# Performance work log

Hardware: AMD Instinct MI355X
Metric: run time of the kernel (lower is better)

Reference implementation:

```python
import jax, jax.numpy as jnp
import numpy as np

B, L, D = 16384, 50, 64      # nodes, history length, embed_dim
NU, NI, NR = 100000, 100000, 5


def setup_inputs() -> dict:
    key = jax.random.key(0)
    ks = jax.random.split(key, 16)
    s = 0.05
    return {
        "nodes": jax.random.randint(ks[0], (B,), 0, NU),
        "history_uv": jax.random.randint(ks[1], (B, L), 0, NI),
        "history_r": jax.random.randint(ks[2], (B, L), 0, NR),
        "v2e_w": jax.random.normal(ks[3], (NI, D), jnp.float32) * s,
        "u2e_w": jax.random.normal(ks[4], (NU, D), jnp.float32) * s,
        "r2e_w": jax.random.normal(ks[5], (NR, D), jnp.float32) * s,
        "w_r1_w": jax.random.normal(ks[6], (2 * D, D), jnp.float32) * s,
        "w_r1_b": jnp.zeros((D,), jnp.float32),
        "w_r2_w": jax.random.normal(ks[7], (D, D), jnp.float32) * s,
        "w_r2_b": jnp.zeros((D,), jnp.float32),
        "att1_w": jax.random.normal(ks[8], (2 * D, D), jnp.float32) * s,
        "att1_b": jnp.zeros((D,), jnp.float32),
        "att2_w": jax.random.normal(ks[9], (D, D), jnp.float32) * s,
        "att2_b": jnp.zeros((D,), jnp.float32),
        "att3_w": jax.random.normal(ks[10], (D, 1), jnp.float32) * s,
        "att3_b": jnp.zeros((1,), jnp.float32),
    }


def reference(nodes, history_uv, history_r, v2e_w, u2e_w, r2e_w,
              w_r1_w, w_r1_b, w_r2_w, w_r2_b,
              att1_w, att1_b, att2_w, att2_b, att3_w, att3_b):
    # Gather neighbor (item) and rating embeddings: [B, L, D]
    e_uv = v2e_w[history_uv]
    e_r = r2e_w[history_r]
    uv_rep = u2e_w[nodes]                      # [B, D] self (user) embedding
    # 2-layer MLP on concatenated (item, rating) embeddings
    x = jnp.concatenate([e_uv, e_r], axis=-1)  # [B, L, 2D]
    h = jax.nn.relu(x @ w_r1_w + w_r1_b)
    o_history = jax.nn.relu(h @ w_r2_w + w_r2_b)  # [B, L, D]
    # Attention over neighbors (GraphRec Attention, dropout off in eval)
    a = jnp.concatenate(
        [o_history, jnp.broadcast_to(uv_rep[:, None, :], o_history.shape)], axis=-1)
    a = jax.nn.relu(a @ att1_w + att1_b)
    a = jax.nn.relu(a @ att2_w + att2_b)
    logits = (a @ att3_w + att3_b)[..., 0]     # [B, L]
    att = jax.nn.softmax(logits, axis=-1)      # softmax over history dim
    # Attention-weighted sum of neighbor representations
    return jnp.einsum('bl,bld->bd', att, o_history)  # [B, D]
```

## Files before the change

kernel.cpp:

```cpp
#include <hip/hip_runtime.h>
#include <math.h>

#define NB 16384
#define LH 50
#define D  64

#define TBF_OFF 49152
#define UB_OFF  65536
#define P1_OFF  4259840

typedef _Float16 half2v __attribute__((ext_vector_type(2)));
typedef _Float16 half8  __attribute__((ext_vector_type(8)));
typedef float    f32x16 __attribute__((ext_vector_type(16)));
typedef unsigned int u32;

#define MFMA(a, b, c) __builtin_amdgcn_mfma_f32_32x32x16_f16((a), (b), (c), 0, 0, 0)


__device__ __forceinline__ u32 pack2(float a, float b) {
    half2v h; h[0] = (_Float16)a; h[1] = (_Float16)b;
    return __builtin_bit_cast(u32, h);
}
__device__ __forceinline__ half8 mk8(u32 a, u32 b, u32 c, u32 d) {
    uint4 t = make_uint4(a, b, c, d);
    return __builtin_bit_cast(half8, t);
}
__device__ __forceinline__ half8 cvt8(const float* __restrict__ p) {
    float4 u = *(const float4*)p;
    float4 v = *(const float4*)(p + 4);
    return mk8(pack2(u.x, u.y), pack2(u.z, u.w), pack2(v.x, v.y), pack2(v.z, v.w));
}
__device__ __forceinline__ half8 addrelu8(half8 a, half8 r) {
    half8 s = a + r;
    #pragma unroll
    for (int j = 0; j < 8; ++j) s[j] = s[j] > (_Float16)0 ? s[j] : (_Float16)0;
    return s;
}

__device__ __forceinline__ void xform_tile(const f32x16& t, int hv, half8& f0, half8& f1) {
    u32 p[8], rp[8];
    #pragma unroll
    for (int q = 0; q < 8; ++q) p[q] = pack2(fmaxf(t[2*q], 0.f), fmaxf(t[2*q+1], 0.f));
    #pragma unroll
    for (int q = 0; q < 8; ++q) rp[q] = (u32)__shfl_xor((int)p[q], 32, 64);
    f0 = hv ? mk8(rp[2], rp[3], p[2], p[3]) : mk8(p[0], p[1], rp[0], rp[1]);
    f1 = hv ? mk8(rp[6], rp[7], p[6], p[7]) : mk8(p[4], p[5], rp[4], rp[5]);
}

__device__ __forceinline__ f32x16 ldbias(const float* tb, int hv, int mt) {
    const float4* p = (const float4*)tb + hv*8 + mt*4;
    f32x16 r;
    #pragma unroll
    for (int q = 0; q < 4; ++q) {
        float4 v = p[q];
        r[4*q] = v.x; r[4*q+1] = v.y; r[4*q+2] = v.z; r[4*q+3] = v.w;
    }
    return r;
}

__device__ __forceinline__ half8 mkw(const float* __restrict__ W, int ks, int mt,
                                     int hv, int m) {
    half8 r;
    #pragma unroll
    for (int j = 0; j < 8; ++j)
        r[j] = (_Float16)W[(ks*16 + hv*8 + j)*64 + mt*32 + m];
    return r;
}

__global__ __launch_bounds__(256) void prep_all(
    const int*   __restrict__ nodes,
    const float* __restrict__ v2e, const float* __restrict__ u2e,
    const float* __restrict__ r2e,
    const float* __restrict__ w1,  const float* __restrict__ b1,
    const float* __restrict__ w2,  const float* __restrict__ b2,
    const float* __restrict__ wa1, const float* __restrict__ ba1,
    const float* __restrict__ wa2, const float* __restrict__ ba2,
    const float* __restrict__ wa3,
    _Float16* __restrict__ wsh, float* __restrict__ tbf,
    float* __restrict__ UB, _Float16* __restrict__ P1h) {
    const int blk = blockIdx.x;
    const int lane = threadIdx.x & 63;
    const int n = lane & 31, hv = lane >> 5;

    if (blk < 782) {
        const int tile = blk*4 + (threadIdx.x >> 6);
        if (tile >= 3125) return;
        const int item = tile*32 + n;
        half8 bf[4];
        #pragma unroll
        for (int ks = 0; ks < 4; ++ks)
            bf[ks] = cvt8(v2e + (size_t)item*64 + ks*16 + hv*8);
        f32x16 a0, a1;
        #pragma unroll
        for (int q = 0; q < 16; ++q) { a0[q] = 0.f; a1[q] = 0.f; }
        #pragma unroll
        for (int ks = 0; ks < 4; ++ks) {
            a0 = MFMA(mkw(w1, ks, 0, hv, n), bf[ks], a0);
            a1 = MFMA(mkw(w1, ks, 1, hv, n), bf[ks], a1);
        }
        u32 dw[16];
        #pragma unroll
        for (int q = 0; q < 8; ++q) dw[q]     = pack2(a0[2*q], a0[2*q+1]);
        #pragma unroll
        for (int q = 0; q < 8; ++q) dw[8 + q] = pack2(a1[2*q], a1[2*q+1]);
        uint4* dst = (uint4*)(P1h + (size_t)item*64 + hv*32);
        dst[0] = make_uint4(dw[0],  dw[1],  dw[2],  dw[3]);
        dst[1] = make_uint4(dw[4],  dw[5],  dw[6],  dw[7]);
        dst[2] = make_uint4(dw[8],  dw[9],  dw[10], dw[11]);
        dst[3] = make_uint4(dw[12], dw[13], dw[14], dw[15]);
        return;
    }
    if (blk < 910) {
        const int tile = (blk - 782)*4 + (threadIdx.x >> 6);
        const int s = tile*32 + n;
        const int nid = nodes[s];
        half8 bf[4];
        #pragma unroll
        for (int ks = 0; ks < 4; ++ks)
            bf[ks] = cvt8(u2e + (size_t)nid*64 + ks*16 + hv*8);
        f32x16 a0, a1;
        #pragma unroll
        for (int q = 0; q < 16; ++q) {
            a0[q] = ba1[(q & 3) + 8*(q >> 2) + 4*hv];
            a1[q] = ba1[32 + (q & 3) + 8*(q >> 2) + 4*hv];
        }
        const float* wup = wa1 + 64*64;
        #pragma unroll
        for (int ks = 0; ks < 4; ++ks) {
            a0 = MFMA(mkw(wup, ks, 0, hv, n), bf[ks], a0);
            a1 = MFMA(mkw(wup, ks, 1, hv, n), bf[ks], a1);
        }
        float4* dst = (float4*)(UB + (size_t)s*64 + hv*32);
        #pragma unroll
        for (int q = 0; q < 4; ++q) {
            dst[q]     = make_float4(a0[4*q], a0[4*q+1], a0[4*q+2], a0[4*q+3]);
            dst[4 + q] = make_float4(a1[4*q], a1[4*q+1], a1[4*q+2], a1[4*q+3]);
        }
        return;
    }
    if (blk < 958) {
        const int idx = (blk - 910)*256 + threadIdx.x;
        const int j = idx & 7, l2 = (idx >> 3) & 63;
        const int hv2 = l2 >> 5, m31 = l2 & 31;
        const int f = (idx >> 9) & 7, ks = f & 3, mt = f >> 2;
        const int sec = idx >> 12;
        const int tau = ks*16 + hv2*8 + j;
        float v;
        if (sec == 0) {
            const int thv = (tau >> 5) & 1, tmt = (tau >> 4) & 1, i = tau & 15;
            const int feat = tmt*32 + (i & 3) + 8*(i >> 2) + 4*thv;
            v = w2[feat*64 + mt*32 + m31];
        }
        else if (sec == 1) v = wa1[tau*64 + mt*32 + m31];
        else               v = wa2[tau*64 + mt*32 + m31];
        wsh[idx] = (_Float16)v;
        return;
    }
    if (blk == 958) {
        if (threadIdx.x < 64) {
            const int t = threadIdx.x;
            const int thv = t >> 5, r = t & 31, mtt = r >> 4, i = r & 15;
            const int feat = mtt*32 + (i & 3) + 8*(i >> 2) + 4*thv;
            tbf[t]       = b2[feat];
            tbf[64 + t]  = ba2[feat];
            tbf[128 + t] = wa3[feat];
        }
        return;
    }
    {
        _Float16* R1h = (_Float16*)(tbf + 192);
        #pragma unroll 1
        for (int base = 0; base < 320; base += 256) {
            const int o = base + (int)threadIdx.x;
            if (o < 320) {
                const int rr = o >> 6, tt = o & 63;
                const int thv = tt >> 5, r5 = tt & 31, mtt = r5 >> 4, i = r5 & 15;
                const int feat = mtt*32 + (i & 3) + 8*(i >> 2) + 4*thv;
                float acc = b1[feat];
                for (int k = 0; k < 64; ++k)
                    acc += r2e[rr*64 + k] * w1[(64 + k)*64 + feat];
                R1h[rr*64 + tt] = (_Float16)acc;
            }
        }
    }
}

__global__ __launch_bounds__(256, 4) void uv_main(
    const int*   __restrict__ huv,
    const int*   __restrict__ hr,
    const _Float16* __restrict__ P1h,
    const float* __restrict__ UB,
    const _Float16* __restrict__ wsh,
    const float* __restrict__ tbf,
    float*       __restrict__ out) {
    __shared__ _Float16 lw[12288];
    __shared__ float    ltb[192];
    __shared__ _Float16 lr1[5*72];
    const int tid = threadIdx.x;

    {
        const uint4* src = (const uint4*)wsh;
        uint4* dst = (uint4*)lw;
        #pragma unroll
        for (int i = 0; i < 6; ++i) dst[tid + 256*i] = src[tid + 256*i];
        if (tid < 48) ((uint4*)ltb)[tid] = ((const uint4*)tbf)[tid];
        if (tid < 40) {
            const int r = tid >> 3, q = tid & 7;
            ((uint4*)lr1)[r*9 + q] = ((const uint4*)(tbf + 192))[tid];
        }
    }
    __syncthreads();

    const int lane = tid & 63;
    const int w = tid >> 6;
    const int b = blockIdx.x * 4 + w;
    const int n = lane & 31, hv = lane >> 5;

    #define G8(base, f) (*(const half8*)(lw + (base) + ((f)*64 + lane)*8))

    const int t1   = (32 + n < LH) ? 32 + n : LH - 1;
    const int row0 = huv[b*LH + n];
    const int row1 = huv[b*LH + t1];
    const int ir0  = hr[b*LH + n];
    const int ir1  = hr[b*LH + t1];

    half8 bf[2][4];
    #pragma unroll
    for (int ks = 0; ks < 4; ++ks) {
        half8 p0 = *(const half8*)(P1h + (size_t)row0*64 + ks*16 + hv*8);
        half8 p1 = *(const half8*)(P1h + (size_t)row1*64 + ks*16 + hv*8);
        half8 r0 = *(const half8*)(lr1 + ir0*72 + ks*16 + hv*8);
        half8 r1 = *(const half8*)(lr1 + ir1*72 + ks*16 + hv*8);
        bf[0][ks] = addrelu8(p0, r0);
        bf[1][ks] = addrelu8(p1, r1);
    }

    half8 of[2][4];
    #pragma unroll
    for (int mt = 0; mt < 2; ++mt) {
        f32x16 a0 = ldbias(ltb, hv, mt);
        f32x16 a1 = ldbias(ltb, hv, mt);
        #pragma unroll
        for (int ks = 0; ks < 4; ++ks) {
            half8 wv = G8(0, mt*4 + ks);
            a0 = MFMA(wv, bf[0][ks], a0);
            a1 = MFMA(wv, bf[1][ks], a1);
        }
        xform_tile(a0, hv, of[0][mt*2], of[0][mt*2 + 1]);
        xform_tile(a1, hv, of[1][mt*2], of[1][mt*2 + 1]);
    }

    const float* ubrow = UB + (size_t)b * 64;
    half8 af[2][4];
    #pragma unroll
    for (int mt = 0; mt < 2; ++mt) {
        f32x16 a0 = ldbias(ubrow, hv, mt);
        f32x16 a1 = ldbias(ubrow, hv, mt);
        #pragma unroll
        for (int ks = 0; ks < 4; ++ks) {
            half8 wv = G8(4096, mt*4 + ks);
            a0 = MFMA(wv, of[0][ks], a0);
            a1 = MFMA(wv, of[1][ks], a1);
        }
        xform_tile(a0, hv, af[0][mt*2], af[0][mt*2 + 1]);
        xform_tile(a1, hv, af[1][mt*2], af[1][mt*2 + 1]);
    }

    float lg0 = 0.f, lg1 = 0.f;
    #pragma unroll
    for (int mt = 0; mt < 2; ++mt) {
        f32x16 c0, c1v;
        {
            const f32x16 bc = ldbias(ltb + 64, hv, mt);
            half8 wv = G8(8192, mt*4 + 0);
            c0  = MFMA(wv, af[0][0], bc);
            c1v = MFMA(wv, af[1][0], bc);
        }
        #pragma unroll
        for (int ks = 1; ks < 4; ++ks) {
            half8 wv = G8(8192, mt*4 + ks);
            c0  = MFMA(wv, af[0][ks], c0);
            c1v = MFMA(wv, af[1][ks], c1v);
        }
        #pragma unroll
        for (int q = 0; q < 4; ++q) {
            float4 w3 = ((const float4*)(ltb + 128))[hv*8 + mt*4 + q];
            lg0 += fmaxf(c0[4*q], 0.f)*w3.x + fmaxf(c0[4*q+1], 0.f)*w3.y
                 + fmaxf(c0[4*q+2], 0.f)*w3.z + fmaxf(c0[4*q+3], 0.f)*w3.w;
            lg1 += fmaxf(c1v[4*q], 0.f)*w3.x + fmaxf(c1v[4*q+1], 0.f)*w3.y
                 + fmaxf(c1v[4*q+2], 0.f)*w3.z + fmaxf(c1v[4*q+3], 0.f)*w3.w;
        }
    }
    lg0 += __shfl_xor(lg0, 32, 64);
    lg1 += __shfl_xor(lg1, 32, 64);
    if (32 + n >= LH) lg1 = -1e30f;

    float mx = fmaxf(lg0, lg1);
    #pragma unroll
    for (int off = 16; off >= 1; off >>= 1) mx = fmaxf(mx, __shfl_xor(mx, off, 64));
    const float e0 = __expf(lg0 - mx);
    const float e1 = __expf(lg1 - mx);
    float s = e0 + e1;
    #pragma unroll
    for (int off = 16; off >= 1; off >>= 1) s += __shfl_xor(s, off, 64);
    const float at0 = e0 / s, at1 = e1 / s;

    float cur[32];
    #pragma unroll
    for (int ks = 0; ks < 4; ++ks)
        #pragma unroll
        for (int j = 0; j < 8; ++j)
            cur[ks*8 + j] = at0 * (float)of[0][ks][j] + at1 * (float)of[1][ks][j];
    #pragma unroll
    for (int k = 0; k < 5; ++k) {
        const int d = 1 << k, mybit = (lane >> k) & 1, half = 16 >> k;
        #pragma unroll
        for (int j2 = 0; j2 < 16; ++j2) {
            if (j2 < half) {
                float sel  = mybit ? cur[2*j2]     : cur[2*j2 + 1];
                float got  = __shfl_xor(sel, d, 64);
                float keep = mybit ? cur[2*j2 + 1] : cur[2*j2];
                cur[j2] = keep + got;
            }
        }
    }
    const int feat = ((lane >> 3) & 3)*16 + hv*8 + (lane & 7);
    __builtin_nontemporal_store(cur[0], out + (size_t)b * D + feat);
    #undef G8
}

extern "C" void kernel_launch(void* const* d_in, const int* in_sizes, int n_in,
                              void* d_out, int out_size, void* d_ws, size_t ws_size,
                              hipStream_t stream) {
    const int*   nodes      = (const int*)  d_in[0];
    const int*   history_uv = (const int*)  d_in[1];
    const int*   history_r  = (const int*)  d_in[2];
    const float* v2e        = (const float*)d_in[3];
    const float* u2e        = (const float*)d_in[4];
    const float* r2e        = (const float*)d_in[5];
    const float* w1         = (const float*)d_in[6];
    const float* b1         = (const float*)d_in[7];
    const float* w2         = (const float*)d_in[8];
    const float* b2         = (const float*)d_in[9];
    const float* wa1        = (const float*)d_in[10];
    const float* ba1        = (const float*)d_in[11];
    const float* wa2        = (const float*)d_in[12];
    const float* ba2        = (const float*)d_in[13];
    const float* wa3        = (const float*)d_in[14];
    float* out = (float*)d_out;

    _Float16* wsh = (_Float16*)d_ws;
    float*    tbf = (float*)((char*)d_ws + TBF_OFF);
    float*    UB  = (float*)((char*)d_ws + UB_OFF);
    _Float16* P1h = (_Float16*)((char*)d_ws + P1_OFF);

    prep_all<<<960, 256, 0, stream>>>(nodes, v2e, u2e, r2e, w1, b1, w2, b2,
                                      wa1, ba1, wa2, ba2, wa3, wsh, tbf, UB, P1h);
    uv_main<<<NB/4, 256, 0, stream>>>(history_uv, history_r,
                                      P1h, UB, wsh, tbf, out);
}
```

Before: 170.4 us.

## Permute feature order in weights to drop cross-lane shuffles; use 512-thread blocks

Precomputed weights, the P1 table and the output index are re-permuted so the MFMA accumulator layout can feed the next MFMA directly. This removes the __shfl_xor lane-swap in each tile transform. The main kernel also moves from 4 to 8 waves per block, so each block does half as many shared-memory weight loads per node and the grid halves. Correctness depends on every permutation matching. Launch bounds of 512×4 may raise register pressure.

```diff
diff --git a/kernel.cpp b/kernel.cpp
--- a/kernel.cpp
+++ b/kernel.cpp
@@ -17,6 +17,11 @@
 #define MFMA(a, b, c) __builtin_amdgcn_mfma_f32_32x32x16_f16((a), (b), (c), 0, 0, 0)
 
 
+__device__ __forceinline__ int featn(int s) {
+    const int ks = s >> 4, hvv = (s >> 3) & 1, j = s & 7;
+    return (ks >> 1)*32 + (ks & 1)*16 + (j & 3) + 8*(j >> 2) + 4*hvv;
+}
+
 __device__ __forceinline__ u32 pack2(float a, float b) {
     half2v h; h[0] = (_Float16)a; h[1] = (_Float16)b;
     return __builtin_bit_cast(u32, h);
@@ -37,14 +42,12 @@
     return s;
 }
 
-__device__ __forceinline__ void xform_tile(const f32x16& t, int hv, half8& f0, half8& f1) {
-    u32 p[8], rp[8];
+__device__ __forceinline__ void xform2(const f32x16& t, half8& f0, half8& f1) {
+    u32 p[8];
     #pragma unroll
     for (int q = 0; q < 8; ++q) p[q] = pack2(fmaxf(t[2*q], 0.f), fmaxf(t[2*q+1], 0.f));
-    #pragma unroll
-    for (int q = 0; q < 8; ++q) rp[q] = (u32)__shfl_xor((int)p[q], 32, 64);
-    f0 = hv ? mk8(rp[2], rp[3], p[2], p[3]) : mk8(p[0], p[1], rp[0], rp[1]);
-    f1 = hv ? mk8(rp[6], rp[7], p[6], p[7]) : mk8(p[4], p[5], rp[4], rp[5]);
+    f0 = mk8(p[0], p[1], p[2], p[3]);
+    f1 = mk8(p[4], p[5], p[6], p[7]);
 }
 
 __device__ __forceinline__ f32x16 ldbias(const float* tb, int hv, int mt) {
@@ -103,11 +106,11 @@
         for (int q = 0; q < 8; ++q) dw[q]     = pack2(a0[2*q], a0[2*q+1]);
         #pragma unroll
         for (int q = 0; q < 8; ++q) dw[8 + q] = pack2(a1[2*q], a1[2*q+1]);
-        uint4* dst = (uint4*)(P1h + (size_t)item*64 + hv*32);
-        dst[0] = make_uint4(dw[0],  dw[1],  dw[2],  dw[3]);
-        dst[1] = make_uint4(dw[4],  dw[5],  dw[6],  dw[7]);
-        dst[2] = make_uint4(dw[8],  dw[9],  dw[10], dw[11]);
-        dst[3] = make_uint4(dw[12], dw[13], dw[14], dw[15]);
+        _Float16* rp = P1h + (size_t)item*64 + hv*8;
+        *(uint4*)(rp)      = make_uint4(dw[0],  dw[1],  dw[2],  dw[3]);
+        *(uint4*)(rp + 16) = make_uint4(dw[4],  dw[5],  dw[6],  dw[7]);
+        *(uint4*)(rp + 32) = make_uint4(dw[8],  dw[9],  dw[10], dw[11]);
+        *(uint4*)(rp + 48) = make_uint4(dw[12], dw[13], dw[14], dw[15]);
         return;
     }
     if (blk < 910) {
@@ -145,14 +148,11 @@
         const int f = (idx >> 9) & 7, ks = f & 3, mt = f >> 2;
         const int sec = idx >> 12;
         const int tau = ks*16 + hv2*8 + j;
+        const int fin = featn(tau);
         float v;
-        if (sec == 0) {
-            const int thv = (tau >> 5) & 1, tmt = (tau >> 4) & 1, i = tau & 15;
-            const int feat = tmt*32 + (i & 3) + 8*(i >> 2) + 4*thv;
-            v = w2[feat*64 + mt*32 + m31];
-        }
-        else if (sec == 1) v = wa1[tau*64 + mt*32 + m31];
-        else               v = wa2[tau*64 + mt*32 + m31];
+        if      (sec == 0) v = w2 [fin*64 + mt*32 + m31];
+        else if (sec == 1) v = wa1[fin*64 + mt*32 + m31];
+        else               v = wa2[fin*64 + mt*32 + m31];
         wsh[idx] = (_Float16)v;
         return;
     }
@@ -174,8 +174,7 @@
             const int o = base + (int)threadIdx.x;
             if (o < 320) {
                 const int rr = o >> 6, tt = o & 63;
-                const int thv = tt >> 5, r5 = tt & 31, mtt = r5 >> 4, i = r5 & 15;
-                const int feat = mtt*32 + (i & 3) + 8*(i >> 2) + 4*thv;
+                const int feat = featn(tt);
                 float acc = b1[feat];
                 for (int k = 0; k < 64; ++k)
                     acc += r2e[rr*64 + k] * w1[(64 + k)*64 + feat];
@@ -185,7 +184,7 @@
     }
 }
 
-__global__ __launch_bounds__(256, 4) void uv_main(
+__global__ __launch_bounds__(512, 4) void uv_main(
     const int*   __restrict__ huv,
     const int*   __restrict__ hr,
     const _Float16* __restrict__ P1h,
@@ -202,7 +201,7 @@
         const uint4* src = (const uint4*)wsh;
         uint4* dst = (uint4*)lw;
         #pragma unroll
-        for (int i = 0; i < 6; ++i) dst[tid + 256*i] = src[tid + 256*i];
+        for (int i = 0; i < 3; ++i) dst[tid + 512*i] = src[tid + 512*i];
         if (tid < 48) ((uint4*)ltb)[tid] = ((const uint4*)tbf)[tid];
         if (tid < 40) {
             const int r = tid >> 3, q = tid & 7;
@@ -213,7 +212,7 @@
 
     const int lane = tid & 63;
     const int w = tid >> 6;
-    const int b = blockIdx.x * 4 + w;
+    const int b = blockIdx.x * 8 + w;
     const int n = lane & 31, hv = lane >> 5;
 
     #define G8(base, f) (*(const half8*)(lw + (base) + ((f)*64 + lane)*8))
@@ -246,8 +245,8 @@
             a0 = MFMA(wv, bf[0][ks], a0);
             a1 = MFMA(wv, bf[1][ks], a1);
         }
-        xform_tile(a0, hv, of[0][mt*2], of[0][mt*2 + 1]);
-        xform_tile(a1, hv, of[1][mt*2], of[1][mt*2 + 1]);
+        xform2(a0, of[0][mt*2], of[0][mt*2 + 1]);
+        xform2(a1, of[1][mt*2], of[1][mt*2 + 1]);
     }
 
     const float* ubrow = UB + (size_t)b * 64;
@@ -262,8 +261,8 @@
             a0 = MFMA(wv, of[0][ks], a0);
             a1 = MFMA(wv, of[1][ks], a1);
         }
-        xform_tile(a0, hv, af[0][mt*2], af[0][mt*2 + 1]);
-        xform_tile(a1, hv, af[1][mt*2], af[1][mt*2 + 1]);
+        xform2(a0, af[0][mt*2], af[0][mt*2 + 1]);
+        xform2(a1, af[1][mt*2], af[1][mt*2 + 1]);
     }
 
     float lg0 = 0.f, lg1 = 0.f;
@@ -324,7 +323,8 @@
             }
         }
     }
-    const int feat = ((lane >> 3) & 3)*16 + hv*8 + (lane & 7);
+    const int ksf = (lane >> 3) & 3, jf = lane & 7;
+    const int feat = (ksf >> 1)*32 + (ksf & 1)*16 + (jf & 3) + 8*(jf >> 2) + 4*hv;
     __builtin_nontemporal_store(cur[0], out + (size_t)b * D + feat);
     #undef G8
 }
@@ -356,6 +356,6 @@
 
     prep_all<<<960, 256, 0, stream>>>(nodes, v2e, u2e, r2e, w1, b1, w2, b2,
                                       wa1, ba1, wa2, ba2, wa3, wsh, tbf, UB, P1h);
-    uv_main<<<NB/4, 256, 0, stream>>>(history_uv, history_r,
+    uv_main<<<NB/8, 512, 0, stream>>>(history_uv, history_r,
                                       P1h, UB, wsh, tbf, out);
 }
```

After: 223.9 us. 1.31x slower.
